# Optimization experiments

Measured on AMD Instinct MI355X. Metric: run time of the kernel, lower is better.

## Reference

```python
import jax, jax.numpy as jnp
import numpy as np

B, L, D, F = 8, 1024, 256, 11
TEMP = D ** 0.5
LN_EPS = 1e-6


def setup_inputs() -> dict:
    key = jax.random.key(0)
    ks = jax.random.split(key, 14)
    mk = lambda k, s: jax.random.normal(k, s, dtype=jnp.float32)
    return {
        "q": mk(ks[0], (B, L, D)),
        "k": mk(ks[1], (B, L, D)),
        "v": mk(ks[2], (B, L, D)),
        "x": jax.random.uniform(ks[3], (B, L, F), dtype=jnp.float32),
        "inputs_lengths": jax.random.randint(ks[4], (B,), 512, L + 1),
        "w_qs": mk(ks[5], (D, D)) * 0.05,
        "w_ks": mk(ks[6], (D, D)) * 0.05,
        "w_vs": mk(ks[7], (D, D)) * 0.05,
        "w_qs2": mk(ks[8], (D, D)) * 0.05,
        "w_ks2": mk(ks[9], (D, D)) * 0.05,
        "w_fc": mk(ks[10], (D, D)) * 0.05,
        "feature_importance": mk(ks[11], (F,)) * 0.1,
        "ln_gamma": jnp.ones((D,), jnp.float32),
        "ln_beta": jnp.zeros((D,), jnp.float32),
    }


def reference(q, k, v, x, w_qs, w_ks, w_vs, w_qs2, w_ks2, w_fc,
              feature_importance, ln_gamma, ln_beta, inputs_lengths):
    lin = lambda a, w: jnp.einsum('bli,oi->blo', a, w)  # torch Linear: y = x W^T
    qp = lin(q, w_qs)
    kp = lin(k, w_ks)
    vp = lin(v, w_vs)
    q2 = lin(q, w_qs2)
    k2 = lin(k, w_ks2)

    # key-position validity mask [B, L]
    key_mask = jnp.arange(L)[None, :] < inputs_lengths[:, None]

    # FeatureSim: pairwise L1 feature distances weighted by feature_importance
    fd = jnp.abs(x[:, :, None, :] - x[:, None, :, :])           # [B,L,L,F]
    fa = jnp.einsum('bijf,f->bij', fd, feature_importance)      # [B,L,L]
    fa = jnp.where(key_mask[:, None, :], fa, -jnp.inf)          # pad_masking
    fa = jax.nn.softmax(fa, axis=-1)
    fa = jnp.nan_to_num(fa)                                     # nan -> 0 for fully-masked rows

    # dual-score attention with tanh activation (no row normalization)
    attn = jnp.einsum('bid,bjd->bij', qp / TEMP, kp)
    q2f = jnp.einsum('bij,bjd->bid', fa, q2)
    k2f = jnp.einsum('bij,bjd->bid', fa, k2)
    attn = attn + jnp.einsum('bid,bjd->bij', q2f / TEMP, k2f)
    zm = key_mask[:, None, :]
    attn = jnp.where(zm, attn, 0.0)                             # pad_zero_masking
    attn = jnp.tanh(attn)
    attn = jnp.where(zm, attn, 0.0)                             # pad_zero_masking (tanh(0)=0, kept for fidelity)

    out = jnp.einsum('bij,bjd->bid', attn, vp)
    out = lin(out, w_fc) + q                                    # dropout is identity at eval
    mu = jnp.mean(out, axis=-1, keepdims=True)
    var = jnp.var(out, axis=-1, keepdims=True)
    out = (out - mu) / jnp.sqrt(var + LN_EPS) * ln_gamma + ln_beta
    return (out, attn)
```

## Files before the change

### kernel.cpp

```cpp
#include <hip/hip_runtime.h>
#include <hip/hip_bf16.h>
#include <math.h>

typedef __hip_bfloat16 bf16;
typedef __bf16 bf16x8 __attribute__((ext_vector_type(8)));
typedef float  f32x4  __attribute__((ext_vector_type(4)));

#define NB 8
#define SL 1024
#define DD 256
#define NF 11
#define RPB 8

#define AS_G __attribute__((address_space(1)))
#define AS_L __attribute__((address_space(3)))

__device__ __forceinline__ bf16x8 ldfrag(const bf16* p) {
  return *reinterpret_cast<const bf16x8*>(p);
}
__device__ __forceinline__ bf16x8 ldfrag(const float* p) {
  const float4 a = *reinterpret_cast<const float4*>(p);
  const float4 b = *reinterpret_cast<const float4*>(p + 4);
  bf16x8 r;
  r[0] = (__bf16)a.x; r[1] = (__bf16)a.y; r[2] = (__bf16)a.z; r[3] = (__bf16)a.w;
  r[4] = (__bf16)b.x; r[5] = (__bf16)b.y; r[6] = (__bf16)b.z; r[7] = (__bf16)b.w;
  return r;
}
__device__ __forceinline__ unsigned short us(float f) {
  bf16 h = __float2bfloat16(f);
  return *reinterpret_cast<unsigned short*>(&h);
}

__device__ __forceinline__ void stage_any(const float* __restrict__ g, int ld,
                                          bf16* __restrict__ s, int tid) {
#pragma unroll
  for (int it = 0; it < 4; ++it) {
    const int cid = it * 256 + tid;
    const int row = cid >> 3, c16 = cid & 7;
    bf16x8 v = ldfrag(g + (size_t)row * ld + c16 * 8);
    *reinterpret_cast<bf16x8*>(s + row * 64 + ((c16 ^ (row & 7)) << 3)) = v;
  }
}

__device__ __forceinline__ void stage_any(const bf16* __restrict__ g, int ld,
                                          bf16* __restrict__ s, int tid) {
  const int wbase = tid & ~63;
#pragma unroll
  for (int it = 0; it < 4; ++it) {
    const int cid = it * 256 + tid;
    const int row = cid >> 3, sc = cid & 7;
    const int c16 = sc ^ (row & 7);
    const bf16* src = g + (size_t)row * ld + c16 * 8;
    bf16* dst = s + (size_t)(it * 256 + wbase) * 8;
    __builtin_amdgcn_global_load_lds((const AS_G void*)src, (AS_L void*)dst, 16, 0, 0);
  }
}

__device__ __forceinline__ void compute_tiles(const bf16* __restrict__ sA,
                                              const bf16* __restrict__ sB,
                                              int lane, int wave, f32x4 acc[4][4]) {
  const int n15 = lane & 15, quad = lane >> 4;
  const int wm = (wave >> 1) * 64, wn = (wave & 1) * 64;
#pragma unroll
  for (int kc = 0; kc < 2; ++kc) {
    const int c16 = kc * 4 + quad;
    bf16x8 aF[4], bF[4];
#pragma unroll
    for (int t = 0; t < 4; ++t) {
      const int ra = wm + t * 16 + n15;
      aF[t] = *reinterpret_cast<const bf16x8*>(sA + ra * 64 + ((c16 ^ (ra & 7)) << 3));
      const int rb = wn + t * 16 + n15;
      bF[t] = *reinterpret_cast<const bf16x8*>(sB + rb * 64 + ((c16 ^ (rb & 7)) << 3));
    }
#pragma unroll
    for (int ti = 0; ti < 4; ++ti)
#pragma unroll
      for (int tj = 0; tj < 4; ++tj)
        acc[ti][tj] = __builtin_amdgcn_mfma_f32_16x16x32_bf16(aF[ti], bF[tj], acc[ti][tj], 0, 0, 0);
  }
}

template<typename TA, typename TB>
__device__ __forceinline__ void gemm_core(const TA* __restrict__ A, int lda,
                                          const TB* __restrict__ B, int ldb, int K,
                                          bf16* sA, bf16* sB, int tid, f32x4 acc[4][4]) {
  const int lane = tid & 63, wave = tid >> 6;
  for (int k0 = 0; k0 < K; k0 += 64) {
    stage_any(A + k0, lda, sA, tid);
    stage_any(B + k0, ldb, sB, tid);
    __syncthreads();
    compute_tiles(sA, sB, lane, wave, acc);
    __syncthreads();
  }
}

__device__ __forceinline__ float wred_sum(float v) {
#pragma unroll
  for (int o = 32; o > 0; o >>= 1) v += __shfl_xor(v, o, 64);
  return v;
}

__global__ __launch_bounds__(256) void k_proj(
    const float* __restrict__ q, const float* __restrict__ k, const float* __restrict__ v,
    const float* __restrict__ wqs, const float* __restrict__ wks, const float* __restrict__ wvs,
    const float* __restrict__ wqs2, const float* __restrict__ wks2,
    bf16* __restrict__ qp, bf16* __restrict__ kp,
    bf16* __restrict__ vpt, bf16* __restrict__ q2t, bf16* __restrict__ k2t)
{
  __shared__ bf16 sA[128 * 64], sB[128 * 64];
  const int tid = threadIdx.x, lane = tid & 63, wave = tid >> 6;
  const int z = blockIdx.z;
  const float* A = (z == 2) ? v : ((z == 1 || z == 4) ? k : q);
  const float* W = (z == 0) ? wqs : (z == 1) ? wks : (z == 2) ? wvs : (z == 3) ? wqs2 : wks2;
  const int rowBase = blockIdx.x * 128;
  const int colBase = blockIdx.y * 128;
  f32x4 acc[4][4] = {};
  gemm_core(A + (size_t)rowBase * DD, DD, W + (size_t)colBase * DD, DD, DD, sA, sB, tid, acc);
  const int n15 = lane & 15, quad = lane >> 4;
  const int wm = (wave >> 1) * 64, wn = (wave & 1) * 64;
  if (z <= 1) {
    bf16* O = (z == 0) ? qp : kp;
#pragma unroll
    for (int ti = 0; ti < 4; ++ti)
#pragma unroll
      for (int tj = 0; tj < 4; ++tj)
#pragma unroll
        for (int r = 0; r < 4; ++r) {
          int row = rowBase + wm + ti * 16 + quad * 4 + r;
          int col = colBase + wn + tj * 16 + n15;
          O[(size_t)row * DD + col] = __float2bfloat16(acc[ti][tj][r]);
        }
  } else {
    bf16* O = (z == 2) ? vpt : (z == 3) ? q2t : k2t;
    const int bb = rowBase >> 10, rowInB = rowBase & 1023;
#pragma unroll
    for (int ti = 0; ti < 4; ++ti)
#pragma unroll
      for (int tj = 0; tj < 4; ++tj) {
        int l0  = rowInB + wm + ti * 16 + quad * 4;
        int col = colBase + wn + tj * 16 + n15;
        ushort4 pk = make_ushort4(us(acc[ti][tj][0]), us(acc[ti][tj][1]),
                                  us(acc[ti][tj][2]), us(acc[ti][tj][3]));
        *reinterpret_cast<ushort4*>(&O[((size_t)bb * DD + col) * SL + l0]) = pk;
      }
  }
}

__global__ __launch_bounds__(256) void k_fa(const float* __restrict__ x,
                                            const float* __restrict__ fi_g,
                                            const int* __restrict__ lens,
                                            bf16* __restrict__ fa)
{
  __shared__ __align__(16) float sx[SL * NF];
  __shared__ float sredS[4][RPB];
  const int tid = threadIdx.x, wave = tid >> 6;
  const int b  = blockIdx.x >> 7;
  const int i0 = (blockIdx.x & 127) * RPB;
  {
    const float4* src = reinterpret_cast<const float4*>(x + (size_t)b * SL * NF);
    float4* dst = reinterpret_cast<float4*>(sx);
#pragma unroll
    for (int it = 0; it < 11; ++it) dst[it * 256 + tid] = src[it * 256 + tid];
  }
  float fiv[NF];
#pragma unroll
  for (int f = 0; f < NF; ++f) fiv[f] = fi_g[f];
  const int len = lens[b];
  __syncthreads();
  float xi[RPB][NF];
#pragma unroll
  for (int i = 0; i < RPB; ++i)
#pragma unroll
    for (int f = 0; f < NF; ++f) xi[i][f] = sx[(i0 + i) * NF + f];
  float e[RPB][4];
  float ps[RPB];
#pragma unroll
  for (int i = 0; i < RPB; ++i) ps[i] = 0.f;
#pragma unroll
  for (int t = 0; t < 4; ++t) {
    const int j = tid + t * 256;
    const bool valid = (t < 2) || (j < len);
    float xj[NF];
#pragma unroll
    for (int f = 0; f < NF; ++f) xj[f] = sx[j * NF + f];
#pragma unroll
    for (int i = 0; i < RPB; ++i) {
      float a = 0.f;
#pragma unroll
      for (int f = 0; f < NF; ++f) a += fabsf(xi[i][f] - xj[f]) * fiv[f];
      float ev = valid ? __expf(a) : 0.f;
      e[i][t] = ev;
      ps[i] += ev;
    }
  }
#pragma unroll
  for (int i = 0; i < RPB; ++i) {
    float wsv = wred_sum(ps[i]);
    if ((tid & 63) == 0) sredS[wave][i] = wsv;
  }
  __syncthreads();
  bf16* out = fa + (size_t)b * SL * SL + (size_t)i0 * SL;
#pragma unroll
  for (int i = 0; i < RPB; ++i) {
    const float inv = 1.f / (sredS[0][i] + sredS[1][i] + sredS[2][i] + sredS[3][i]);
#pragma unroll
    for (int t = 0; t < 4; ++t)
      out[(size_t)i * SL + tid + t * 256] = __float2bfloat16(e[i][t] * inv);
  }
}

__global__ __launch_bounds__(256) void k_famul(const bf16* __restrict__ fa,
                                               const bf16* __restrict__ q2t,
                                               const bf16* __restrict__ k2t,
                                               bf16* __restrict__ q2f,
                                               bf16* __restrict__ k2f)
{
  __shared__ bf16 sA[128 * 64], sB[128 * 64];
  const int tid = threadIdx.x, lane = tid & 63, wave = tid >> 6;
  const int b = blockIdx.z >> 1, which = blockIdx.z & 1;
  const int iBase = blockIdx.x * 128, dBase = blockIdx.y * 128;
  const bf16* A  = fa + (size_t)b * SL * SL + (size_t)iBase * SL;
  const bf16* Bm = (which ? k2t : q2t) + (size_t)b * DD * SL + (size_t)dBase * SL;
  f32x4 acc[4][4] = {};
  gemm_core(A, SL, Bm, SL, SL, sA, sB, tid, acc);
  bf16* O = (which ? k2f : q2f) + (size_t)b * SL * DD;
  const int n15 = lane & 15, quad = lane >> 4;
  const int wm = (wave >> 1) * 64, wn = (wave & 1) * 64;
#pragma unroll
  for (int ti = 0; ti < 4; ++ti)
#pragma unroll
    for (int tj = 0; tj < 4; ++tj)
#pragma unroll
      for (int r = 0; r < 4; ++r)
        O[(size_t)(iBase + wm + ti * 16 + quad * 4 + r) * DD +
          dBase + wn + tj * 16 + n15] = __float2bfloat16(acc[ti][tj][r]);
}

__global__ __launch_bounds__(256) void k_attn(const bf16* __restrict__ qp,
                                              const bf16* __restrict__ kp,
                                              const bf16* __restrict__ q2f,
                                              const bf16* __restrict__ k2f,
                                              const int* __restrict__ lens,
                                              float* __restrict__ attn_f32,
                                              bf16* __restrict__ attn_b16)
{
  __shared__ bf16 sA[128 * 64], sB[128 * 64];
  const int tid = threadIdx.x, lane = tid & 63, wave = tid >> 6;
  const int b = blockIdx.z;
  const int iBase = blockIdx.x * 128, jBase = blockIdx.y * 128;
  f32x4 acc[4][4] = {};
  gemm_core(qp  + ((size_t)b * SL + iBase) * DD, DD,
            kp  + ((size_t)b * SL + jBase) * DD, DD, DD, sA, sB, tid, acc);
  gemm_core(q2f + ((size_t)b * SL + iBase) * DD, DD,
            k2f + ((size_t)b * SL + jBase) * DD, DD, DD, sA, sB, tid, acc);
  const int len = lens[b];
  const int n15 = lane & 15, quad = lane >> 4;
  const int wm = (wave >> 1) * 64, wn = (wave & 1) * 64;
#pragma unroll
  for (int ti = 0; ti < 4; ++ti)
#pragma unroll
    for (int tj = 0; tj < 4; ++tj)
#pragma unroll
      for (int r = 0; r < 4; ++r) {
        int i = iBase + wm + ti * 16 + quad * 4 + r;
        int j = jBase + wn + tj * 16 + n15;
        float vv = (j < len) ? tanhf(acc[ti][tj][r] * (1.f / 16.f)) : 0.f;
        size_t idx = (size_t)b * SL * SL + (size_t)i * SL + j;
        attn_f32[idx] = vv;
        attn_b16[idx] = __float2bfloat16(vv);
      }
}

__global__ __launch_bounds__(256) void k_av(const bf16* __restrict__ attn,
                                            const bf16* __restrict__ vpt,
                                            bf16* __restrict__ out_pre)
{
  __shared__ bf16 sA[128 * 64], sB[128 * 64];
  const int tid = threadIdx.x, lane = tid & 63, wave = tid >> 6;
  const int b = blockIdx.z;
  const int iBase = blockIdx.x * 128, dBase = blockIdx.y * 128;
  f32x4 acc[4][4] = {};
  gemm_core(attn + (size_t)b * SL * SL + (size_t)iBase * SL, SL,
            vpt  + (size_t)b * DD * SL + (size_t)dBase * SL, SL, SL, sA, sB, tid, acc);
  bf16* O = out_pre + (size_t)b * SL * DD;
  const int n15 = lane & 15, quad = lane >> 4;
  const int wm = (wave >> 1) * 64, wn = (wave & 1) * 64;
#pragma unroll
  for (int ti = 0; ti < 4; ++ti)
#pragma unroll
    for (int tj = 0; tj < 4; ++tj)
#pragma unroll
      for (int r = 0; r < 4; ++r)
        O[(size_t)(iBase + wm + ti * 16 + quad * 4 + r) * DD +
          dBase + wn + tj * 16 + n15] = __float2bfloat16(acc[ti][tj][r]);
}

__global__ __launch_bounds__(256) void k_fc(const bf16* __restrict__ out_pre,
                                            const float* __restrict__ wfc,
                                            const float* __restrict__ qres,
                                            float* __restrict__ fcout)
{
  __shared__ bf16 sA[128 * 64], sB[128 * 64];
  const int tid = threadIdx.x, lane = tid & 63, wave = tid >> 6;
  const int rowBase = blockIdx.x * 128, colBase = blockIdx.y * 128;
  f32x4 acc[4][4] = {};
  gemm_core(out_pre + (size_t)rowBase * DD, DD, wfc + (size_t)colBase * DD, DD, DD,
            sA, sB, tid, acc);
  const int n15 = lane & 15, quad = lane >> 4;
  const int wm = (wave >> 1) * 64, wn = (wave & 1) * 64;
#pragma unroll
  for (int ti = 0; ti < 4; ++ti)
#pragma unroll
    for (int tj = 0; tj < 4; ++tj)
#pragma unroll
      for (int r = 0; r < 4; ++r) {
        int row = rowBase + wm + ti * 16 + quad * 4 + r;
        int col = colBase + wn + tj * 16 + n15;
        fcout[(size_t)row * DD + col] = acc[ti][tj][r] + qres[(size_t)row * DD + col];
      }
}

__global__ __launch_bounds__(256) void k_ln(const float* __restrict__ fcout,
                                            const float* __restrict__ gam,
                                            const float* __restrict__ bet,
                                            float* __restrict__ outp)
{
  __shared__ float r1[4], r2[4];
  const int r = blockIdx.x, tid = threadIdx.x;
  const float v = fcout[(size_t)r * DD + tid];
  float s = wred_sum(v), ss = wred_sum(v * v);
  if ((tid & 63) == 0) { r1[tid >> 6] = s; r2[tid >> 6] = ss; }
  __syncthreads();
  s  = r1[0] + r1[1] + r1[2] + r1[3];
  ss = r2[0] + r2[1] + r2[2] + r2[3];
  const float mean = s * (1.f / DD);
  const float var  = ss * (1.f / DD) - mean * mean;
  float y = (v - mean) * rsqrtf(var + 1e-6f);
  y = y * gam[tid] + bet[tid];
  outp[(size_t)r * DD + tid] = y;
}

extern "C" void kernel_launch(void* const* d_in, const int* in_sizes, int n_in,
                              void* d_out, int out_size, void* d_ws, size_t ws_size,
                              hipStream_t stream)
{
  const float* q    = (const float*)d_in[0];
  const float* k    = (const float*)d_in[1];
  const float* v    = (const float*)d_in[2];
  const float* x    = (const float*)d_in[3];
  const int*  lens  = (const int*)d_in[4];
  const float* wqs  = (const float*)d_in[5];
  const float* wks  = (const float*)d_in[6];
  const float* wvs  = (const float*)d_in[7];
  const float* wqs2 = (const float*)d_in[8];
  const float* wks2 = (const float*)d_in[9];
  const float* wfc  = (const float*)d_in[10];
  const float* fi   = (const float*)d_in[11];
  const float* gam  = (const float*)d_in[12];
  const float* bet  = (const float*)d_in[13];

  char* w = (char*)d_ws;
  const size_t MB = 1u << 20;
  bf16* qp   = (bf16*)(w + 0 * MB);
  bf16* kp   = (bf16*)(w + 4 * MB);
  bf16* vpt  = (bf16*)(w + 8 * MB);
  bf16* q2t  = (bf16*)(w + 12 * MB);
  bf16* k2t  = (bf16*)(w + 16 * MB);
  bf16* q2f  = (bf16*)(w + 20 * MB);
  bf16* k2f  = (bf16*)(w + 24 * MB);
  bf16* fa   = (bf16*)(w + 28 * MB);
  bf16* attn_b16 = fa;
  bf16* out_pre = q2t;
  float* fcout  = (float*)(w + 0 * MB);

  float* outp  = (float*)d_out;
  float* attnp = outp + (size_t)NB * SL * DD;

  dim3 blk(256);
  hipLaunchKernelGGL(k_proj,  dim3(64, 2, 5),  blk, 0, stream,
                     q, k, v, wqs, wks, wvs, wqs2, wks2, qp, kp, vpt, q2t, k2t);
  hipLaunchKernelGGL(k_fa,    dim3(NB * 128),  blk, 0, stream, x, fi, lens, fa);
  hipLaunchKernelGGL(k_famul, dim3(8, 2, 16),  blk, 0, stream, fa, q2t, k2t, q2f, k2f);
  hipLaunchKernelGGL(k_attn,  dim3(8, 8, 8),   blk, 0, stream,
                     qp, kp, q2f, k2f, lens, attnp, attn_b16);
  hipLaunchKernelGGL(k_av,    dim3(8, 2, 8),   blk, 0, stream, attn_b16, vpt, out_pre);
  hipLaunchKernelGGL(k_fc,    dim3(64, 2),     blk, 0, stream, out_pre, wfc, q, fcout);
  hipLaunchKernelGGL(k_ln,    dim3(NB * SL),   blk, 0, stream, fcout, gam, bet, outp);
}
```

Measured before the change: 217.9 us.

## Double-buffer GEMM LDS staging, concatenate attention operands, remap blocks across XCDs

The shared GEMM core now uses two LDS buffers, issuing the global loads for the next K tile before computing the current one and dropping one barrier per iteration. The Q/K projections and their feature-weighted variants are written side by side into 512-wide concatenated buffers, so the attention kernel runs one K=512 GEMM instead of two K=256 passes. The famul, attn and av kernels also remap their flat block index so that neighbouring tiles of the same batch sit on the same XCD, aiming for better L2 reuse. LDS per block doubles to 64KB, which may lower occupancy.

```diff
diff --git a/kernel.cpp b/kernel.cpp
--- a/kernel.cpp
+++ b/kernel.cpp
@@ -83,14 +83,21 @@
 template<typename TA, typename TB>
 __device__ __forceinline__ void gemm_core(const TA* __restrict__ A, int lda,
                                           const TB* __restrict__ B, int ldb, int K,
-                                          bf16* sA, bf16* sB, int tid, f32x4 acc[4][4]) {
+                                          bf16* s, int tid, f32x4 acc[4][4]) {
   const int lane = tid & 63, wave = tid >> 6;
+  bf16* bufA[2] = { s,         s + 16384 };
+  bf16* bufB[2] = { s + 8192,  s + 24576 };
+  stage_any(A, lda, bufA[0], tid);
+  stage_any(B, ldb, bufB[0], tid);
+  int cur = 0;
   for (int k0 = 0; k0 < K; k0 += 64) {
-    stage_any(A + k0, lda, sA, tid);
-    stage_any(B + k0, ldb, sB, tid);
     __syncthreads();
-    compute_tiles(sA, sB, lane, wave, acc);
-    __syncthreads();
+    if (k0 + 64 < K) {
+      stage_any(A + k0 + 64, lda, bufA[cur ^ 1], tid);
+      stage_any(B + k0 + 64, ldb, bufB[cur ^ 1], tid);
+    }
+    compute_tiles(bufA[cur], bufB[cur], lane, wave, acc);
+    cur ^= 1;
   }
 }
 
@@ -104,10 +111,10 @@
     const float* __restrict__ q, const float* __restrict__ k, const float* __restrict__ v,
     const float* __restrict__ wqs, const float* __restrict__ wks, const float* __restrict__ wvs,
     const float* __restrict__ wqs2, const float* __restrict__ wks2,
-    bf16* __restrict__ qp, bf16* __restrict__ kp,
+    bf16* __restrict__ qq, bf16* __restrict__ kk,
     bf16* __restrict__ vpt, bf16* __restrict__ q2t, bf16* __restrict__ k2t)
 {
-  __shared__ bf16 sA[128 * 64], sB[128 * 64];
+  __shared__ bf16 smem[4 * 128 * 64];
   const int tid = threadIdx.x, lane = tid & 63, wave = tid >> 6;
   const int z = blockIdx.z;
   const float* A = (z == 2) ? v : ((z == 1 || z == 4) ? k : q);
@@ -115,11 +122,11 @@
   const int rowBase = blockIdx.x * 128;
   const int colBase = blockIdx.y * 128;
   f32x4 acc[4][4] = {};
-  gemm_core(A + (size_t)rowBase * DD, DD, W + (size_t)colBase * DD, DD, DD, sA, sB, tid, acc);
+  gemm_core(A + (size_t)rowBase * DD, DD, W + (size_t)colBase * DD, DD, DD, smem, tid, acc);
   const int n15 = lane & 15, quad = lane >> 4;
   const int wm = (wave >> 1) * 64, wn = (wave & 1) * 64;
   if (z <= 1) {
-    bf16* O = (z == 0) ? qp : kp;
+    bf16* O = (z == 0) ? qq : kk;
 #pragma unroll
     for (int ti = 0; ti < 4; ++ti)
 #pragma unroll
@@ -128,7 +135,7 @@
         for (int r = 0; r < 4; ++r) {
           int row = rowBase + wm + ti * 16 + quad * 4 + r;
           int col = colBase + wn + tj * 16 + n15;
-          O[(size_t)row * DD + col] = __float2bfloat16(acc[ti][tj][r]);
+          O[(size_t)row * 512 + col] = __float2bfloat16(acc[ti][tj][r]);
         }
   } else {
     bf16* O = (z == 2) ? vpt : (z == 3) ? q2t : k2t;
@@ -212,18 +219,21 @@
 __global__ __launch_bounds__(256) void k_famul(const bf16* __restrict__ fa,
                                                const bf16* __restrict__ q2t,
                                                const bf16* __restrict__ k2t,
-                                               bf16* __restrict__ q2f,
-                                               bf16* __restrict__ k2f)
-{
-  __shared__ bf16 sA[128 * 64], sB[128 * 64];
-  const int tid = threadIdx.x, lane = tid & 63, wave = tid >> 6;
-  const int b = blockIdx.z >> 1, which = blockIdx.z & 1;
-  const int iBase = blockIdx.x * 128, dBase = blockIdx.y * 128;
+                                               bf16* __restrict__ qq,
+                                               bf16* __restrict__ kk)
+{
+  __shared__ bf16 smem[4 * 128 * 64];
+  const int tid = threadIdx.x, lane = tid & 63, wave = tid >> 6;
+  const int flat = blockIdx.x + 8 * blockIdx.y + 16 * blockIdx.z;
+  const int lid  = (flat & 7) * 32 + (flat >> 3);
+  const int bx = lid & 7, by = (lid >> 3) & 1, bz = lid >> 4;
+  const int b = bz >> 1, which = bz & 1;
+  const int iBase = bx * 128, dBase = by * 128;
   const bf16* A  = fa + (size_t)b * SL * SL + (size_t)iBase * SL;
   const bf16* Bm = (which ? k2t : q2t) + (size_t)b * DD * SL + (size_t)dBase * SL;
   f32x4 acc[4][4] = {};
-  gemm_core(A, SL, Bm, SL, SL, sA, sB, tid, acc);
-  bf16* O = (which ? k2f : q2f) + (size_t)b * SL * DD;
+  gemm_core(A, SL, Bm, SL, SL, smem, tid, acc);
+  bf16* O = (which ? kk : qq) + (size_t)b * SL * 512 + 256;
   const int n15 = lane & 15, quad = lane >> 4;
   const int wm = (wave >> 1) * 64, wn = (wave & 1) * 64;
 #pragma unroll
@@ -232,27 +242,26 @@
     for (int tj = 0; tj < 4; ++tj)
 #pragma unroll
       for (int r = 0; r < 4; ++r)
-        O[(size_t)(iBase + wm + ti * 16 + quad * 4 + r) * DD +
+        O[(size_t)(iBase + wm + ti * 16 + quad * 4 + r) * 512 +
           dBase + wn + tj * 16 + n15] = __float2bfloat16(acc[ti][tj][r]);
 }
 
-__global__ __launch_bounds__(256) void k_attn(const bf16* __restrict__ qp,
-                                              const bf16* __restrict__ kp,
-                                              const bf16* __restrict__ q2f,
-                                              const bf16* __restrict__ k2f,
+__global__ __launch_bounds__(256) void k_attn(const bf16* __restrict__ qq,
+                                              const bf16* __restrict__ kk,
                                               const int* __restrict__ lens,
                                               float* __restrict__ attn_f32,
                                               bf16* __restrict__ attn_b16)
 {
-  __shared__ bf16 sA[128 * 64], sB[128 * 64];
-  const int tid = threadIdx.x, lane = tid & 63, wave = tid >> 6;
-  const int b = blockIdx.z;
-  const int iBase = blockIdx.x * 128, jBase = blockIdx.y * 128;
-  f32x4 acc[4][4] = {};
-  gemm_core(qp  + ((size_t)b * SL + iBase) * DD, DD,
-            kp  + ((size_t)b * SL + jBase) * DD, DD, DD, sA, sB, tid, acc);
-  gemm_core(q2f + ((size_t)b * SL + iBase) * DD, DD,
-            k2f + ((size_t)b * SL + jBase) * DD, DD, DD, sA, sB, tid, acc);
+  __shared__ bf16 smem[4 * 128 * 64];
+  const int tid = threadIdx.x, lane = tid & 63, wave = tid >> 6;
+  const int flat = blockIdx.x + 8 * blockIdx.y + 64 * blockIdx.z;
+  const int lid  = (flat & 7) * 64 + (flat >> 3);
+  const int bx = lid & 7, by = (lid >> 3) & 7, bz = lid >> 6;
+  const int b = bz;
+  const int iBase = bx * 128, jBase = by * 128;
+  f32x4 acc[4][4] = {};
+  gemm_core(qq + ((size_t)b * SL + iBase) * 512, 512,
+            kk + ((size_t)b * SL + jBase) * 512, 512, 512, smem, tid, acc);
   const int len = lens[b];
   const int n15 = lane & 15, quad = lane >> 4;
   const int wm = (wave >> 1) * 64, wn = (wave & 1) * 64;
@@ -275,13 +284,16 @@
                                             const bf16* __restrict__ vpt,
                                             bf16* __restrict__ out_pre)
 {
-  __shared__ bf16 sA[128 * 64], sB[128 * 64];
-  const int tid = threadIdx.x, lane = tid & 63, wave = tid >> 6;
-  const int b = blockIdx.z;
-  const int iBase = blockIdx.x * 128, dBase = blockIdx.y * 128;
+  __shared__ bf16 smem[4 * 128 * 64];
+  const int tid = threadIdx.x, lane = tid & 63, wave = tid >> 6;
+  const int flat = blockIdx.x + 8 * blockIdx.y + 16 * blockIdx.z;
+  const int lid  = (flat & 7) * 16 + (flat >> 3);
+  const int bx = lid & 7, by = (lid >> 3) & 1, bz = lid >> 4;
+  const int b = bz;
+  const int iBase = bx * 128, dBase = by * 128;
   f32x4 acc[4][4] = {};
   gemm_core(attn + (size_t)b * SL * SL + (size_t)iBase * SL, SL,
-            vpt  + (size_t)b * DD * SL + (size_t)dBase * SL, SL, SL, sA, sB, tid, acc);
+            vpt  + (size_t)b * DD * SL + (size_t)dBase * SL, SL, SL, smem, tid, acc);
   bf16* O = out_pre + (size_t)b * SL * DD;
   const int n15 = lane & 15, quad = lane >> 4;
   const int wm = (wave >> 1) * 64, wn = (wave & 1) * 64;
@@ -300,12 +312,12 @@
                                             const float* __restrict__ qres,
                                             float* __restrict__ fcout)
 {
-  __shared__ bf16 sA[128 * 64], sB[128 * 64];
+  __shared__ bf16 smem[4 * 128 * 64];
   const int tid = threadIdx.x, lane = tid & 63, wave = tid >> 6;
   const int rowBase = blockIdx.x * 128, colBase = blockIdx.y * 128;
   f32x4 acc[4][4] = {};
   gemm_core(out_pre + (size_t)rowBase * DD, DD, wfc + (size_t)colBase * DD, DD, DD,
-            sA, sB, tid, acc);
+            smem, tid, acc);
   const int n15 = lane & 15, quad = lane >> 4;
   const int wm = (wave >> 1) * 64, wn = (wave & 1) * 64;
 #pragma unroll
@@ -361,13 +373,11 @@
 
   char* w = (char*)d_ws;
   const size_t MB = 1u << 20;
-  bf16* qp   = (bf16*)(w + 0 * MB);
-  bf16* kp   = (bf16*)(w + 4 * MB);
-  bf16* vpt  = (bf16*)(w + 8 * MB);
-  bf16* q2t  = (bf16*)(w + 12 * MB);
-  bf16* k2t  = (bf16*)(w + 16 * MB);
-  bf16* q2f  = (bf16*)(w + 20 * MB);
-  bf16* k2f  = (bf16*)(w + 24 * MB);
+  bf16* qq   = (bf16*)(w + 0 * MB);
+  bf16* kk   = (bf16*)(w + 8 * MB);
+  bf16* vpt  = (bf16*)(w + 16 * MB);
+  bf16* q2t  = (bf16*)(w + 20 * MB);
+  bf16* k2t  = (bf16*)(w + 24 * MB);
   bf16* fa   = (bf16*)(w + 28 * MB);
   bf16* attn_b16 = fa;
   bf16* out_pre = q2t;
@@ -378,11 +388,11 @@
 
   dim3 blk(256);
   hipLaunchKernelGGL(k_proj,  dim3(64, 2, 5),  blk, 0, stream,
-                     q, k, v, wqs, wks, wvs, wqs2, wks2, qp, kp, vpt, q2t, k2t);
+                     q, k, v, wqs, wks, wvs, wqs2, wks2, qq, kk, vpt, q2t, k2t);
   hipLaunchKernelGGL(k_fa,    dim3(NB * 128),  blk, 0, stream, x, fi, lens, fa);
-  hipLaunchKernelGGL(k_famul, dim3(8, 2, 16),  blk, 0, stream, fa, q2t, k2t, q2f, k2f);
+  hipLaunchKernelGGL(k_famul, dim3(8, 2, 16),  blk, 0, stream, fa, q2t, k2t, qq, kk);
   hipLaunchKernelGGL(k_attn,  dim3(8, 8, 8),   blk, 0, stream,
-                     qp, kp, q2f, k2f, lens, attnp, attn_b16);
+                     qq, kk, lens, attnp, attn_b16);
   hipLaunchKernelGGL(k_av,    dim3(8, 2, 8),   blk, 0, stream, attn_b16, vpt, out_pre);
   hipLaunchKernelGGL(k_fc,    dim3(64, 2),     blk, 0, stream, out_pre, wfc, q, fcout);
   hipLaunchKernelGGL(k_ln,    dim3(NB * SL),   blk, 0, stream, fcout, gam, bet, outp);
```

Result: slower. 229.6 us (+5.4%).
